# Kernel optimization log

Hardware: AMD Instinct MI355X
Metric: run time of the kernel (lower is better)

## Reference

```python
import jax, jax.numpy as jnp
import numpy as np

N_HEAD = 12
NUM_BLOCK_TOKENS = 64
SSMAX_S_INIT = 0.43


def setup_inputs() -> dict:
    key = jax.random.key(0)
    k1, k2, k3 = jax.random.split(key, 3)
    B, T, C = 2, 2048, 768
    x = jax.random.normal(k1, (B, T, C), dtype=jnp.float32)
    # torch Linear weights: y = x @ W.T ; init scaled for stability
    c_attn_w = jax.random.normal(k2, (3 * C, C), dtype=jnp.float32) * 0.02
    c_proj_w = jax.random.normal(k3, (C, C), dtype=jnp.float32) * 0.02
    s = jnp.full((1,), SSMAX_S_INIT, dtype=jnp.float32)  # learnable SSMax scale
    return {"x": x, "c_attn_w": c_attn_w, "c_proj_w": c_proj_w, "s": s}


def reference(x, c_attn_w, c_proj_w, s):
    B, T, C = x.shape
    H, hd, n = N_HEAD, C // N_HEAD, NUM_BLOCK_TOKENS
    qkv = x @ c_attn_w.T                              # [B,T,3C]
    q, k, v = jnp.split(qkv, 3, axis=-1)
    q = q.reshape(B, T, H, hd).transpose(0, 2, 1, 3)  # [B,H,T,hd]
    k = k.reshape(B, T, H, hd).transpose(0, 2, 1, 3)
    v = v.reshape(B, T, H, hd).transpose(0, 2, 1, 3)
    att = jnp.einsum('bhqd,bhkd->bhqk', q, k) * (1.0 / np.sqrt(hd))
    # slot-based block mask reduces to block-causal: allow s_idx//n <= t_idx//n
    blk = jnp.arange(T) // n
    mask = blk[:, None] >= blk[None, :]               # [T,T] bool, True=attend
    scale = s[0] * np.log(T).astype(np.float32)       # SSMax: s * log(N)
    att = jnp.where(mask[None, None], att * scale, -jnp.inf)
    att = jax.nn.softmax(att, axis=-1)
    y = jnp.einsum('bhqk,bhkd->bhqd', att, v)
    y = y.transpose(0, 2, 1, 3).reshape(B, T, C)
    return y @ c_proj_w.T
```

## Files before the change

### kernel.cpp

```cpp
#include <hip/hip_runtime.h>
#include <hip/hip_bf16.h>
#include <stdint.h>

#define T_SEQ 2048
#define C_DIM 768
#define NH 12
#define HD 64
#define QK_LD 1536

typedef __attribute__((ext_vector_type(8))) short short8;
typedef __attribute__((ext_vector_type(4))) float f32x4;
typedef const __attribute__((address_space(1))) void* gas_ptr;
typedef __attribute__((address_space(3))) void* las_ptr;

static __device__ __forceinline__ unsigned short f2bf(float f) {
  union { float f; unsigned u; } c; c.f = f;
  unsigned u = c.u + 0x7fffu + ((c.u >> 16) & 1u);
  return (unsigned short)(u >> 16);
}

__global__ void cast3_kernel(const float* __restrict__ a, int na4,
                             const float* __restrict__ b, int nb4,
                             const float* __restrict__ c, int nc4,
                             unsigned short* __restrict__ oa,
                             unsigned short* __restrict__ ob,
                             unsigned short* __restrict__ oc) {
  int i = blockIdx.x * blockDim.x + threadIdx.x;
  int stride = gridDim.x * blockDim.x;
  int total = na4 + nb4 + nc4;
  for (; i < total; i += stride) {
    const float4* src; ushort4* dst; int j;
    if (i < na4)            { src = (const float4*)a; dst = (ushort4*)oa; j = i; }
    else if (i < na4 + nb4) { src = (const float4*)b; dst = (ushort4*)ob; j = i - na4; }
    else                    { src = (const float4*)c; dst = (ushort4*)oc; j = i - na4 - nb4; }
    float4 v = src[j];
    ushort4 o;
    o.x = f2bf(v.x); o.y = f2bf(v.y); o.z = f2bf(v.z); o.w = f2bf(v.w);
    dst[j] = o;
  }
}

template <int NP>
__device__ __forceinline__ void stage_tile(const unsigned short* g, int ld,
                                           unsigned short* ldsbase, int tid) {
#pragma unroll
  for (int p = 0; p < NP; ++p) {
    int j = p * 256 + tid;
    int row = j >> 2, cc = (j & 3) << 3;
    const unsigned short* ga = g + (size_t)row * ld + cc;
    unsigned short* la = ldsbase + p * 2048 + (tid >> 6) * 512;
    __builtin_amdgcn_global_load_lds((gas_ptr)ga, (las_ptr)la, 16, 0, 0);
  }
}

template <int N>
__device__ __forceinline__ void wait_vmcnt() {
  if constexpr (N == 0) asm volatile("s_waitcnt vmcnt(0)" ::: "memory");
  else if constexpr (N == 3) asm volatile("s_waitcnt vmcnt(3)" ::: "memory");
  else if constexpr (N == 6) asm volatile("s_waitcnt vmcnt(6)" ::: "memory");
  else static_assert(N == 0 || N == 3 || N == 6, "add vmcnt literal");
}

template <int BM, int BN, int EPI, int NY, int PERX, int MAXB>
__launch_bounds__(256, MAXB)
__global__ void gemm_bt(const unsigned short* __restrict__ A,
                        const unsigned short* __restrict__ B,
                        int K,
                        unsigned short* __restrict__ obf,
                        unsigned short* __restrict__ vt,
                        float* __restrict__ ofp,
                        const float* __restrict__ sptr) {
  constexpr int MI = BM / 32;
  constexpr int NJ = BN / 32;
  constexpr int NPA = BM / 64, NPB = BN / 64;
  constexpr int S = NPA + NPB;
  constexpr int ABUF = BM * 32;
  constexpr int BUF = ABUF + BN * 32;
  constexpr int LDS_SH = 2 * BUF;
  constexpr int TR_SH = (EPI == 0) ? 128 * 130 : 0;
  constexpr int TOT = LDS_SH > TR_SH ? LDS_SH : TR_SH;
  __shared__ __attribute__((aligned(16))) unsigned short smem[TOT];
  int tid = threadIdx.x;
  int lane = tid & 63, wave = tid >> 6;
  int L = blockIdx.x;
  int t0 = (L & 7) * PERX + (L >> 3);
  int row0 = (t0 / NY) * BM, col0 = (t0 % NY) * BN;
  int wr = (wave >> 1) * (BM / 2), wc = (wave & 1) * (BN / 2);
  int la = lane & 15, lb = lane >> 4;
  f32x4 acc[MI][NJ] = {};

  const unsigned short* Abase = A + (size_t)row0 * K;
  const unsigned short* Bbase = B + (size_t)col0 * K;
  stage_tile<NPA>(Abase, K, smem, tid);
  stage_tile<NPB>(Bbase, K, smem + ABUF, tid);
  int cur = 0;
  int nt = K >> 5;
  for (int t = 0; t < nt; ++t) {
    asm volatile("" ::: "memory");
    __builtin_amdgcn_s_barrier();
    if (t + 1 < nt) {
      stage_tile<NPA>(Abase + (t + 1) * 32, K, smem + (cur ^ 1) * BUF, tid);
      stage_tile<NPB>(Bbase + (t + 1) * 32, K, smem + (cur ^ 1) * BUF + ABUF, tid);
      wait_vmcnt<S>();
    } else {
      wait_vmcnt<0>();
    }
    __builtin_amdgcn_s_barrier();
    asm volatile("" ::: "memory");
    __builtin_amdgcn_sched_barrier(0);

    unsigned short* lds = smem + cur * BUF;
    short8 af[MI], bfr[NJ];
#pragma unroll
    for (int i = 0; i < MI; ++i)
      af[i] = *(const short8*)&lds[(wr + i * 16 + la) * 32 + lb * 8];
#pragma unroll
    for (int j = 0; j < NJ; ++j)
      bfr[j] = *(const short8*)&lds[ABUF + (wc + j * 16 + la) * 32 + lb * 8];
#pragma unroll
    for (int i = 0; i < MI; ++i)
#pragma unroll
      for (int j = 0; j < NJ; ++j)
        acc[i][j] = __builtin_amdgcn_mfma_f32_16x16x32_bf16(af[i], bfr[j], acc[i][j], 0, 0, 0);
    cur ^= 1;
  }

  if (EPI == 0 && col0 >= 1536) {
    __syncthreads();
    int bb = row0 >> 11, t0r = row0 & 2047;
    int cl = tid >> 1, half = tid & 1;
#pragma unroll
    for (int p = 0; p < BN / 128; ++p) {
      if ((wave & 1) == p) {
#pragma unroll
        for (int i = 0; i < MI; ++i)
#pragma unroll
          for (int j = 0; j < NJ; ++j)
#pragma unroll
            for (int r = 0; r < 4; ++r)
              smem[(wr + i * 16 + lb * 4 + r) * 130 + (j * 16 + la)] =
                  f2bf(acc[i][j][r]);
      }
      __syncthreads();
      int vcol = col0 - 1536 + p * 128 + cl;
      int h = vcol >> 6, d = vcol & 63;
      unsigned short* dst =
          vt + ((size_t)(bb * NH + h) * 64 + d) * T_SEQ + t0r + half * 64;
#pragma unroll
      for (int j = 0; j < 8; ++j) {
        short8 v8;
#pragma unroll
        for (int e = 0; e < 8; ++e)
          v8[e] = (short)smem[(half * 64 + j * 8 + e) * 130 + cl];
        *(short8*)(dst + j * 8) = v8;
      }
      __syncthreads();
    }
    return;
  }

  float qs = 0.f;
  if (EPI == 0)
    qs = sptr[0] * 7.624618986159398f  * 0.125f
         * 1.4426950408889634f ;
#pragma unroll
  for (int i = 0; i < MI; ++i) {
    int gr0 = row0 + wr + i * 16 + lb * 4;
#pragma unroll
    for (int j = 0; j < NJ; ++j) {
      int gc = col0 + wc + j * 16 + la;
#pragma unroll
      for (int r = 0; r < 4; ++r) {
        float v = acc[i][j][r];
        int rr = gr0 + r;
        if (EPI == 0) {
          obf[(size_t)rr * QK_LD + gc] = f2bf(gc < 768 ? v * qs : v);
        } else {
          ofp[(size_t)rr * C_DIM + gc] = v;
        }
      }
    }
  }
}

__device__ __forceinline__ void attn_stage(const unsigned short* kg,
                                           const unsigned short* vg,
                                           char* kbuf, int wave, int lane) {
  int l3 = lane >> 3;
  int cg = ((lane & 7) ^ l3) << 4;
#pragma unroll
  for (int q = 0; q < 2; ++q) {
    int rk = q * 32 + wave * 8 + l3;
    const unsigned short* ka = kg + (size_t)rk * QK_LD + (cg >> 1);
    char* kl = kbuf + (q * 32 + wave * 8) * 128;
    __builtin_amdgcn_global_load_lds((gas_ptr)ka, (las_ptr)kl, 16, 0, 0);
    const unsigned short* va = vg + (size_t)rk * T_SEQ + (cg >> 1);
    char* vl = kbuf + 8192 + (q * 32 + wave * 8) * 128;
    __builtin_amdgcn_global_load_lds((gas_ptr)va, (las_ptr)vl, 16, 0, 0);
  }
}

__launch_bounds__(256, 4)
__global__ void attn_kernel(const unsigned short* __restrict__ qkb,
                            const unsigned short* __restrict__ vt,
                            float* __restrict__ yp,
                            float* __restrict__ lsp,
                            unsigned short* __restrict__ yb) {
  __shared__ __attribute__((aligned(16))) char smem[2 * 16384 + 8192];

  int tid = threadIdx.x, lane = tid & 63, wave = tid >> 6;
  int la = lane & 15, lb = lane >> 4;
  int L = blockIdx.x;
  int ixcd = L >> 3;
  int bh = (L & 7) * 3 + ixcd / 48;
  int xx = 47 - (ixcd % 48);
  int qi, cch;
  if (xx < 16) { qi = xx; cch = 0; }
  else         { int t = xx - 16; qi = 16 + (t >> 1); cch = t & 1; }
  int kt0 = cch * 16;
  int kt1 = min(qi, kt0 + 15);
  int b = bh / NH, h = bh - b * NH;

  const unsigned short* qbase =
      qkb + ((size_t)(b * T_SEQ + qi * 64 + wave * 16 + la)) * QK_LD + h * HD;
  short8 qf0 = *(const short8*)(qbase + lb * 8);
  short8 qf1 = *(const short8*)(qbase + 32 + lb * 8);
  asm volatile("" :: "v"(qf0), "v"(qf1));

  f32x4 y[4] = {};
  float ls[4] = {0.f, 0.f, 0.f, 0.f};

  const unsigned short* kg0 = qkb + (size_t)b * T_SEQ * QK_LD + 768 + h * HD;
  const unsigned short* vg0 = vt + (size_t)bh * 64 * T_SEQ;
  char* pw = smem + 32768 + wave * 2048;

  attn_stage(kg0 + (size_t)kt0 * 64 * QK_LD, vg0 + kt0 * 64, smem, wave, lane);
  int cur = 0;

  for (int kt = kt0; kt <= kt1; ++kt) {
    asm volatile("" ::: "memory");
    __builtin_amdgcn_s_barrier();
    if (kt < kt1) {
      attn_stage(kg0 + (size_t)(kt + 1) * 64 * QK_LD, vg0 + (kt + 1) * 64,
                 smem + ((cur ^ 1) * 16384), wave, lane);
      asm volatile("s_waitcnt vmcnt(4)" ::: "memory");
    } else {
      asm volatile("s_waitcnt vmcnt(0)" ::: "memory");
    }
    __builtin_amdgcn_s_barrier();
    asm volatile("" ::: "memory");
    __builtin_amdgcn_sched_barrier(0);

    char* kl = smem + cur * 16384;
    char* vl = kl + 8192;

    f32x4 s[4] = {};
    __builtin_amdgcn_s_setprio(1);
#pragma unroll
    for (int fk = 0; fk < 4; ++fk) {
      int row = fk * 16 + la;
      {
        int off = (row * 128 + 0 * 64 + lb * 16) ^ ((row & 7) << 4);
        short8 kf = *(const short8*)(kl + off);
        s[fk] = __builtin_amdgcn_mfma_f32_16x16x32_bf16(qf0, kf, s[fk], 0, 0, 0);
      }
      {
        int off = (row * 128 + 1 * 64 + lb * 16) ^ ((row & 7) << 4);
        short8 kf = *(const short8*)(kl + off);
        s[fk] = __builtin_amdgcn_mfma_f32_16x16x32_bf16(qf1, kf, s[fk], 0, 0, 0);
      }
    }
    __builtin_amdgcn_s_setprio(0);

#pragma unroll
    for (int fk = 0; fk < 4; ++fk)
#pragma unroll
      for (int r = 0; r < 4; ++r) {
        float p = __builtin_amdgcn_exp2f(s[fk][r]);
        s[fk][r] = p;
        ls[r] += p;
        int row = lb * 4 + r;
        int off = (row * 128 + (fk * 16 + la) * 2) ^ ((row & 7) << 4);
        *(unsigned short*)(pw + off) = f2bf(p);
      }

    short8 pa[2];
#pragma unroll
    for (int ch = 0; ch < 2; ++ch) {
      int off = (la * 128 + ch * 64 + lb * 16) ^ ((la & 7) << 4);
      pa[ch] = *(const short8*)(pw + off);
    }
    __builtin_amdgcn_s_setprio(1);
#pragma unroll
    for (int fd = 0; fd < 4; ++fd) {
      int row = fd * 16 + la;
#pragma unroll
      for (int ch = 0; ch < 2; ++ch) {
        int off = (row * 128 + ch * 64 + lb * 16) ^ ((row & 7) << 4);
        short8 vf = *(const short8*)(vl + off);
        y[fd] = __builtin_amdgcn_mfma_f32_16x16x32_bf16(pa[ch], vf, y[fd], 0, 0, 0);
      }
    }
    __builtin_amdgcn_s_setprio(0);

    cur ^= 1;
  }

#pragma unroll
  for (int r = 0; r < 4; ++r) {
    float v = ls[r];
    v += __shfl_xor(v, 1); v += __shfl_xor(v, 2);
    v += __shfl_xor(v, 4); v += __shfl_xor(v, 8);
    ls[r] = v;
  }
  int trow = qi * 64 + wave * 16 + lb * 4;

  if (qi < 16) {
    float inv[4];
#pragma unroll
    for (int r = 0; r < 4; ++r) inv[r] = 1.0f / ls[r];
#pragma unroll
    for (int fd = 0; fd < 4; ++fd)
#pragma unroll
      for (int r = 0; r < 4; ++r) {
        int rowg = b * T_SEQ + trow + r;
        int colg = h * HD + fd * 16 + la;
        yb[(size_t)rowg * C_DIM + colg] = f2bf(y[fd][r] * inv[r]);
      }
  } else {
    size_t slotbase = (size_t)cch * (24 * 2048);
    if (la == 0) {
#pragma unroll
      for (int r = 0; r < 4; ++r)
        lsp[slotbase + (size_t)bh * 2048 + trow + r] = ls[r];
    }
    float* ydst = yp + (slotbase + (size_t)bh * 2048) * 64;
#pragma unroll
    for (int fd = 0; fd < 4; ++fd)
#pragma unroll
      for (int r = 0; r < 4; ++r)
        ydst[(size_t)(trow + r) * 64 + fd * 16 + la] = y[fd][r];
  }
}

__global__ void norm_kernel(const float* __restrict__ yp,
                            const float* __restrict__ lsp,
                            unsigned short* __restrict__ yb) {
  int gid = blockIdx.x * blockDim.x + threadIdx.x;
  int dq = gid & 15;
  int rloc = gid >> 4;
  int bh = rloc >> 10, t = 1024 + (rloc & 1023);
  int row = bh * 2048 + t;
  int b = bh / NH, h = bh - b * NH;
  float denom = lsp[row] + lsp[24 * 2048 + row];
  float inv = 1.0f / denom;
  float4 y0 = ((const float4*)yp)[row * 16 + dq];
  float4 y1 = ((const float4*)yp)[(24 * 2048 * 16) + row * 16 + dq];
  ushort4 o;
  o.x = f2bf((y0.x + y1.x) * inv);
  o.y = f2bf((y0.y + y1.y) * inv);
  o.z = f2bf((y0.z + y1.z) * inv);
  o.w = f2bf((y0.w + y1.w) * inv);
  ((ushort4*)yb)[(size_t)(b * T_SEQ + t) * 192 + h * 16 + dq] = o;
}

extern "C" void kernel_launch(void* const* d_in, const int* in_sizes, int n_in,
                              void* d_out, int out_size, void* d_ws, size_t ws_size,
                              hipStream_t stream) {
  const float* x = (const float*)d_in[0];
  const float* attn_w = (const float*)d_in[1];
  const float* proj_w = (const float*)d_in[2];
  const float* s = (const float*)d_in[3];
  float* out = (float*)d_out;

  char* ws = (char*)d_ws;
  unsigned short* xb  = (unsigned short*)(ws);
  unsigned short* wab = (unsigned short*)(ws + 6291456);
  unsigned short* wpb = (unsigned short*)(ws + 9830400);
  unsigned short* qkb = (unsigned short*)(ws + 11010048);
  unsigned short* vtb = (unsigned short*)(ws + 23592960);
  unsigned short* yb  = (unsigned short*)(ws + 29884416);
  float*          yp  = (float*)(ws + 36175872);
  float*          lsp = (float*)(ws + 61341696);

  cast3_kernel<<<2048, 256, 0, stream>>>(x, 3145728 / 4, attn_w, 1769472 / 4,
                                         proj_w, 589824 / 4, xb, wab, wpb);

  gemm_bt<128, 256, 0, 9, 36, 2><<<288, 256, 0, stream>>>(xb, wab, 768, qkb, vtb, nullptr, s);

  attn_kernel<<<1152, 256, 0, stream>>>(qkb, vtb, yp, lsp, yb);

  norm_kernel<<<1536, 256, 0, stream>>>(yp, lsp, yb);

  gemm_bt<64, 128, 1, 6, 48, 4><<<384, 256, 0, stream>>>(yb, wpb, 768, nullptr, nullptr, out, nullptr);
}
```

Baseline: 149.8 us.

## Drop split-KV attention and norm kernel; one block per query tile

Measured after the change: 159.6 us. +6.5%, slower.

```diff
diff --git a/kernel.cpp b/kernel.cpp
--- a/kernel.cpp
+++ b/kernel.cpp
@@ -203,8 +203,6 @@
 __launch_bounds__(256, 4)
 __global__ void attn_kernel(const unsigned short* __restrict__ qkb,
                             const unsigned short* __restrict__ vt,
-                            float* __restrict__ yp,
-                            float* __restrict__ lsp,
                             unsigned short* __restrict__ yb) {
   __shared__ __attribute__((aligned(16))) char smem[2 * 16384 + 8192];
 
@@ -212,13 +210,8 @@
   int la = lane & 15, lb = lane >> 4;
   int L = blockIdx.x;
   int ixcd = L >> 3;
-  int bh = (L & 7) * 3 + ixcd / 48;
-  int xx = 47 - (ixcd % 48);
-  int qi, cch;
-  if (xx < 16) { qi = xx; cch = 0; }
-  else         { int t = xx - 16; qi = 16 + (t >> 1); cch = t & 1; }
-  int kt0 = cch * 16;
-  int kt1 = min(qi, kt0 + 15);
+  int bh = (L & 7) * 3 + ixcd / 32;
+  int qi = 31 - (ixcd & 31);
   int b = bh / NH, h = bh - b * NH;
 
   const unsigned short* qbase =
@@ -234,13 +227,13 @@
   const unsigned short* vg0 = vt + (size_t)bh * 64 * T_SEQ;
   char* pw = smem + 32768 + wave * 2048;
 
-  attn_stage(kg0 + (size_t)kt0 * 64 * QK_LD, vg0 + kt0 * 64, smem, wave, lane);
+  attn_stage(kg0, vg0, smem, wave, lane);
   int cur = 0;
 
-  for (int kt = kt0; kt <= kt1; ++kt) {
+  for (int kt = 0; kt <= qi; ++kt) {
     asm volatile("" ::: "memory");
     __builtin_amdgcn_s_barrier();
-    if (kt < kt1) {
+    if (kt < qi) {
       attn_stage(kg0 + (size_t)(kt + 1) * 64 * QK_LD, vg0 + (kt + 1) * 64,
                  smem + ((cur ^ 1) * 16384), wave, lane);
       asm volatile("s_waitcnt vmcnt(4)" ::: "memory");
@@ -311,57 +304,17 @@
     float v = ls[r];
     v += __shfl_xor(v, 1); v += __shfl_xor(v, 2);
     v += __shfl_xor(v, 4); v += __shfl_xor(v, 8);
-    ls[r] = v;
+    ls[r] = 1.0f / v;
   }
   int trow = qi * 64 + wave * 16 + lb * 4;
-
-  if (qi < 16) {
-    float inv[4];
-#pragma unroll
-    for (int r = 0; r < 4; ++r) inv[r] = 1.0f / ls[r];
-#pragma unroll
-    for (int fd = 0; fd < 4; ++fd)
-#pragma unroll
-      for (int r = 0; r < 4; ++r) {
-        int rowg = b * T_SEQ + trow + r;
-        int colg = h * HD + fd * 16 + la;
-        yb[(size_t)rowg * C_DIM + colg] = f2bf(y[fd][r] * inv[r]);
-      }
-  } else {
-    size_t slotbase = (size_t)cch * (24 * 2048);
-    if (la == 0) {
-#pragma unroll
-      for (int r = 0; r < 4; ++r)
-        lsp[slotbase + (size_t)bh * 2048 + trow + r] = ls[r];
-    }
-    float* ydst = yp + (slotbase + (size_t)bh * 2048) * 64;
-#pragma unroll
-    for (int fd = 0; fd < 4; ++fd)
-#pragma unroll
-      for (int r = 0; r < 4; ++r)
-        ydst[(size_t)(trow + r) * 64 + fd * 16 + la] = y[fd][r];
-  }
-}
-
-__global__ void norm_kernel(const float* __restrict__ yp,
-                            const float* __restrict__ lsp,
-                            unsigned short* __restrict__ yb) {
-  int gid = blockIdx.x * blockDim.x + threadIdx.x;
-  int dq = gid & 15;
-  int rloc = gid >> 4;
-  int bh = rloc >> 10, t = 1024 + (rloc & 1023);
-  int row = bh * 2048 + t;
-  int b = bh / NH, h = bh - b * NH;
-  float denom = lsp[row] + lsp[24 * 2048 + row];
-  float inv = 1.0f / denom;
-  float4 y0 = ((const float4*)yp)[row * 16 + dq];
-  float4 y1 = ((const float4*)yp)[(24 * 2048 * 16) + row * 16 + dq];
-  ushort4 o;
-  o.x = f2bf((y0.x + y1.x) * inv);
-  o.y = f2bf((y0.y + y1.y) * inv);
-  o.z = f2bf((y0.z + y1.z) * inv);
-  o.w = f2bf((y0.w + y1.w) * inv);
-  ((ushort4*)yb)[(size_t)(b * T_SEQ + t) * 192 + h * 16 + dq] = o;
+#pragma unroll
+  for (int fd = 0; fd < 4; ++fd)
+#pragma unroll
+    for (int r = 0; r < 4; ++r) {
+      int rowg = b * T_SEQ + trow + r;
+      int colg = h * HD + fd * 16 + la;
+      yb[(size_t)rowg * C_DIM + colg] = f2bf(y[fd][r] * ls[r]);
+    }
 }
 
 extern "C" void kernel_launch(void* const* d_in, const int* in_sizes, int n_in,
@@ -380,17 +333,13 @@
   unsigned short* qkb = (unsigned short*)(ws + 11010048);
   unsigned short* vtb = (unsigned short*)(ws + 23592960);
   unsigned short* yb  = (unsigned short*)(ws + 29884416);
-  float*          yp  = (float*)(ws + 36175872);
-  float*          lsp = (float*)(ws + 61341696);
 
   cast3_kernel<<<2048, 256, 0, stream>>>(x, 3145728 / 4, attn_w, 1769472 / 4,
                                          proj_w, 589824 / 4, xb, wab, wpb);
 
   gemm_bt<128, 256, 0, 9, 36, 2><<<288, 256, 0, stream>>>(xb, wab, 768, qkb, vtb, nullptr, s);
 
-  attn_kernel<<<1152, 256, 0, stream>>>(qkb, vtb, yp, lsp, yb);
-
-  norm_kernel<<<1536, 256, 0, stream>>>(yp, lsp, yb);
+  attn_kernel<<<768, 256, 0, stream>>>(qkb, vtb, yb);
 
   gemm_bt<64, 128, 1, 6, 48, 4><<<384, 256, 0, stream>>>(yb, wpb, 768, nullptr, nullptr, out, nullptr);
 }
```

## Process two query tiles per attention workgroup to reuse staged K/V tiles

Applied to the files above, without the earlier changes.

After: 171.0 us. +14.1%, slower.

```diff
diff --git a/kernel.cpp b/kernel.cpp
--- a/kernel.cpp
+++ b/kernel.cpp
@@ -212,23 +212,30 @@
   int la = lane & 15, lb = lane >> 4;
   int L = blockIdx.x;
   int ixcd = L >> 3;
-  int bh = (L & 7) * 3 + ixcd / 48;
-  int xx = 47 - (ixcd % 48);
-  int qi, cch;
-  if (xx < 16) { qi = xx; cch = 0; }
-  else         { int t = xx - 16; qi = 16 + (t >> 1); cch = t & 1; }
-  int kt0 = cch * 16;
-  int kt1 = min(qi, kt0 + 15);
+  int bh = (L & 7) * 3 + ixcd / 24;
+  int c0 = ixcd % 24;
+  int c;
+  if (c0 < 8) c = 8 + c0;
+  else { int t = c0 - 8; int pj = 7 - (t >> 1);
+         c = (t & 1) ? pj : 16 + pj; }
+  int qa, qb, kt0, kt1, ctype;
+  if (c < 8)       { qa = 2 * c;            qb = qa + 1; kt0 = 0;  kt1 = qb; ctype = 0; }
+  else if (c < 16) { qa = 16 + 2 * (c - 8); qb = qa + 1; kt0 = 0;  kt1 = 15; ctype = 1; }
+  else             { qa = 16 + 2 * (c - 16); qb = qa + 1; kt0 = 16; kt1 = qb; ctype = 2; }
   int b = bh / NH, h = bh - b * NH;
 
-  const unsigned short* qbase =
-      qkb + ((size_t)(b * T_SEQ + qi * 64 + wave * 16 + la)) * QK_LD + h * HD;
-  short8 qf0 = *(const short8*)(qbase + lb * 8);
-  short8 qf1 = *(const short8*)(qbase + 32 + lb * 8);
-  asm volatile("" :: "v"(qf0), "v"(qf1));
-
-  f32x4 y[4] = {};
-  float ls[4] = {0.f, 0.f, 0.f, 0.f};
+  const unsigned short* qra =
+      qkb + ((size_t)(b * T_SEQ + qa * 64 + wave * 16 + la)) * QK_LD + h * HD;
+  const unsigned short* qrb =
+      qkb + ((size_t)(b * T_SEQ + qb * 64 + wave * 16 + la)) * QK_LD + h * HD;
+  short8 qaf0 = *(const short8*)(qra + lb * 8);
+  short8 qaf1 = *(const short8*)(qra + 32 + lb * 8);
+  short8 qbf0 = *(const short8*)(qrb + lb * 8);
+  short8 qbf1 = *(const short8*)(qrb + 32 + lb * 8);
+  asm volatile("" :: "v"(qaf0), "v"(qaf1), "v"(qbf0), "v"(qbf1));
+
+  f32x4 ya[4] = {}, ybacc[4] = {};
+  float lsa[4] = {0.f, 0.f, 0.f, 0.f}, lsb[4] = {0.f, 0.f, 0.f, 0.f};
 
   const unsigned short* kg0 = qkb + (size_t)b * T_SEQ * QK_LD + 768 + h * HD;
   const unsigned short* vg0 = vt + (size_t)bh * 64 * T_SEQ;
@@ -254,7 +261,7 @@
     char* kl = smem + cur * 16384;
     char* vl = kl + 8192;
 
-    f32x4 s[4] = {};
+    f32x4 sa[4] = {}, sb[4] = {};
     __builtin_amdgcn_s_setprio(1);
 #pragma unroll
     for (int fk = 0; fk < 4; ++fk) {
@@ -262,34 +269,53 @@
       {
         int off = (row * 128 + 0 * 64 + lb * 16) ^ ((row & 7) << 4);
         short8 kf = *(const short8*)(kl + off);
-        s[fk] = __builtin_amdgcn_mfma_f32_16x16x32_bf16(qf0, kf, s[fk], 0, 0, 0);
+        sa[fk] = __builtin_amdgcn_mfma_f32_16x16x32_bf16(qaf0, kf, sa[fk], 0, 0, 0);
+        sb[fk] = __builtin_amdgcn_mfma_f32_16x16x32_bf16(qbf0, kf, sb[fk], 0, 0, 0);
       }
       {
         int off = (row * 128 + 1 * 64 + lb * 16) ^ ((row & 7) << 4);
         short8 kf = *(const short8*)(kl + off);
-        s[fk] = __builtin_amdgcn_mfma_f32_16x16x32_bf16(qf1, kf, s[fk], 0, 0, 0);
+        sa[fk] = __builtin_amdgcn_mfma_f32_16x16x32_bf16(qaf1, kf, sa[fk], 0, 0, 0);
+        sb[fk] = __builtin_amdgcn_mfma_f32_16x16x32_bf16(qbf1, kf, sb[fk], 0, 0, 0);
       }
     }
     __builtin_amdgcn_s_setprio(0);
 
+    float gate = (kt <= qa) ? 1.0f : 0.0f;
+
 #pragma unroll
     for (int fk = 0; fk < 4; ++fk)
 #pragma unroll
       for (int r = 0; r < 4; ++r) {
-        float p = __builtin_amdgcn_exp2f(s[fk][r]);
-        s[fk][r] = p;
-        ls[r] += p;
+        float p = __builtin_amdgcn_exp2f(sa[fk][r]) * gate;
+        lsa[r] += p;
         int row = lb * 4 + r;
         int off = (row * 128 + (fk * 16 + la) * 2) ^ ((row & 7) << 4);
         *(unsigned short*)(pw + off) = f2bf(p);
       }
-
-    short8 pa[2];
+    short8 paa[2];
 #pragma unroll
     for (int ch = 0; ch < 2; ++ch) {
       int off = (la * 128 + ch * 64 + lb * 16) ^ ((la & 7) << 4);
-      pa[ch] = *(const short8*)(pw + off);
-    }
+      paa[ch] = *(const short8*)(pw + off);
+    }
+#pragma unroll
+    for (int fk = 0; fk < 4; ++fk)
+#pragma unroll
+      for (int r = 0; r < 4; ++r) {
+        float p = __builtin_amdgcn_exp2f(sb[fk][r]);
+        lsb[r] += p;
+        int row = lb * 4 + r;
+        int off = (row * 128 + (fk * 16 + la) * 2) ^ ((row & 7) << 4);
+        *(unsigned short*)(pw + off) = f2bf(p);
+      }
+    short8 pab[2];
+#pragma unroll
+    for (int ch = 0; ch < 2; ++ch) {
+      int off = (la * 128 + ch * 64 + lb * 16) ^ ((la & 7) << 4);
+      pab[ch] = *(const short8*)(pw + off);
+    }
+
     __builtin_amdgcn_s_setprio(1);
 #pragma unroll
     for (int fd = 0; fd < 4; ++fd) {
@@ -298,7 +324,8 @@
       for (int ch = 0; ch < 2; ++ch) {
         int off = (row * 128 + ch * 64 + lb * 16) ^ ((row & 7) << 4);
         short8 vf = *(const short8*)(vl + off);
-        y[fd] = __builtin_amdgcn_mfma_f32_16x16x32_bf16(pa[ch], vf, y[fd], 0, 0, 0);
+        ya[fd] = __builtin_amdgcn_mfma_f32_16x16x32_bf16(paa[ch], vf, ya[fd], 0, 0, 0);
+        ybacc[fd] = __builtin_amdgcn_mfma_f32_16x16x32_bf16(pab[ch], vf, ybacc[fd], 0, 0, 0);
       }
     }
     __builtin_amdgcn_s_setprio(0);
@@ -308,38 +335,44 @@
 
 #pragma unroll
   for (int r = 0; r < 4; ++r) {
-    float v = ls[r];
-    v += __shfl_xor(v, 1); v += __shfl_xor(v, 2);
-    v += __shfl_xor(v, 4); v += __shfl_xor(v, 8);
-    ls[r] = v;
-  }
-  int trow = qi * 64 + wave * 16 + lb * 4;
-
-  if (qi < 16) {
-    float inv[4];
-#pragma unroll
-    for (int r = 0; r < 4; ++r) inv[r] = 1.0f / ls[r];
+    float va = lsa[r], vb = lsb[r];
+    va += __shfl_xor(va, 1); va += __shfl_xor(va, 2);
+    va += __shfl_xor(va, 4); va += __shfl_xor(va, 8);
+    vb += __shfl_xor(vb, 1); vb += __shfl_xor(vb, 2);
+    vb += __shfl_xor(vb, 4); vb += __shfl_xor(vb, 8);
+    lsa[r] = va; lsb[r] = vb;
+  }
+  int trowa = qa * 64 + wave * 16 + lb * 4;
+  int trowb = qb * 64 + wave * 16 + lb * 4;
+
+  if (ctype == 0) {
+#pragma unroll
+    for (int r = 0; r < 4; ++r) { lsa[r] = 1.0f / lsa[r]; lsb[r] = 1.0f / lsb[r]; }
 #pragma unroll
     for (int fd = 0; fd < 4; ++fd)
 #pragma unroll
       for (int r = 0; r < 4; ++r) {
-        int rowg = b * T_SEQ + trow + r;
         int colg = h * HD + fd * 16 + la;
-        yb[(size_t)rowg * C_DIM + colg] = f2bf(y[fd][r] * inv[r]);
+        yb[(size_t)(b * T_SEQ + trowa + r) * C_DIM + colg] = f2bf(ya[fd][r] * lsa[r]);
+        yb[(size_t)(b * T_SEQ + trowb + r) * C_DIM + colg] = f2bf(ybacc[fd][r] * lsb[r]);
       }
   } else {
-    size_t slotbase = (size_t)cch * (24 * 2048);
+    size_t slotbase = (size_t)(ctype - 1) * (24 * 2048);
     if (la == 0) {
 #pragma unroll
-      for (int r = 0; r < 4; ++r)
-        lsp[slotbase + (size_t)bh * 2048 + trow + r] = ls[r];
+      for (int r = 0; r < 4; ++r) {
+        lsp[slotbase + (size_t)bh * 2048 + trowa + r] = lsa[r];
+        lsp[slotbase + (size_t)bh * 2048 + trowb + r] = lsb[r];
+      }
     }
     float* ydst = yp + (slotbase + (size_t)bh * 2048) * 64;
 #pragma unroll
     for (int fd = 0; fd < 4; ++fd)
 #pragma unroll
-      for (int r = 0; r < 4; ++r)
-        ydst[(size_t)(trow + r) * 64 + fd * 16 + la] = y[fd][r];
+      for (int r = 0; r < 4; ++r) {
+        ydst[(size_t)(trowa + r) * 64 + fd * 16 + la] = ya[fd][r];
+        ydst[(size_t)(trowb + r) * 64 + fd * 16 + la] = ybacc[fd][r];
+      }
   }
 }
 
@@ -388,7 +421,7 @@
 
   gemm_bt<128, 256, 0, 9, 36, 2><<<288, 256, 0, stream>>>(xb, wab, 768, qkb, vtb, nullptr, s);
 
-  attn_kernel<<<1152, 256, 0, stream>>>(qkb, vtb, yp, lsp, yb);
+  attn_kernel<<<576, 256, 0, stream>>>(qkb, vtb, yp, lsp, yb);
 
   norm_kernel<<<1536, 256, 0, stream>>>(yp, lsp, yb);
 
```
